# Performance work log

Measured on AMD Instinct MI355X. Metric: run time of the kernel, lower is better.

The kernel has to match this reference:

```python
import jax, jax.numpy as jnp
import numpy as np

NEG_SLOPE = 0.01  # nn.LeakyReLU default
EM_DIM = 64

def setup_inputs() -> dict:
    key = jax.random.key(0)
    k1, k2, k3, k4, k5 = jax.random.split(key, 5)
    B, N, D = 4, 512, EM_DIM
    embeddings = jax.random.normal(k1, (B, N, D), dtype=jnp.float32)
    # att_W: Linear(D, D) -> weight [D, D], bias [D]
    W_w = jax.random.normal(k2, (D, D), dtype=jnp.float32) * (1.0 / np.sqrt(D))
    W_b = jax.random.normal(k3, (D,), dtype=jnp.float32) * 0.01
    # att_a: Linear(3D, 1) -> weight [3D], bias scalar
    a_w = jax.random.normal(k4, (3 * D,), dtype=jnp.float32) * (1.0 / np.sqrt(3 * D))
    a_b = jax.random.normal(k5, (1,), dtype=jnp.float32) * 0.01
    return {"embeddings": embeddings, "W_w": W_w, "W_b": W_b, "a_w": a_w, "a_b": a_b}

def reference(embeddings, W_w, W_b, a_w, a_b):
    # embeddings: [B, N, D]
    D = embeddings.shape[-1]
    # pairwise elementwise product: value[b,i,j,d] = e[b,i,d] * e[b,j,d]
    value = embeddings[:, :, None, :] * embeddings[:, None, :, :]  # [B,N,N,D]
    # att_W applied to (broadcast) query/key is row/col-constant -> compute once per node
    w_e = jnp.einsum('bnd,ed->bne', embeddings, W_w) + W_b   # [B,N,D] (= wq rows = wk cols)
    wv = jnp.einsum('bijd,ed->bije', value, W_w) + W_b       # [B,N,N,D]
    # att_a on concat(wq, wk, wv): split the weight vector into three D-chunks
    a_q, a_k, a_v = a_w[:D], a_w[D:2*D], a_w[2*D:]
    s_q = w_e @ a_q  # [B,N]
    s_k = w_e @ a_k  # [B,N]
    s = s_q[:, :, None] + s_k[:, None, :] + jnp.einsum('bije,e->bij', wv, a_v) + a_b[0]  # [B,N,N]
    s = jnp.where(s >= 0, s, NEG_SLOPE * s)  # LeakyReLU; dropout is identity in eval
    alphas = jax.nn.softmax(s, axis=-1)[..., None]  # [B,N,N,1]
    return alphas, value
```

## Files before the change

kernel.cpp:

```cpp
#include <hip/hip_runtime.h>

#define DD 64
#define NN 512
#define BB 4
#define NEG_SLOPE 0.01f

typedef float floatx4 __attribute__((ext_vector_type(4)));

__global__ void precompute_kernel(const float* __restrict__ W_w,
                                  const float* __restrict__ W_b,
                                  const float* __restrict__ a_w,
                                  const float* __restrict__ a_b,
                                  float* __restrict__ ws) {
    int d = threadIdx.x;
    float cq = 0.f, ck = 0.f, cv = 0.f;
    for (int e = 0; e < DD; ++e) {
        float w = W_w[e * DD + d];
        cq = fmaf(a_w[e], w, cq);
        ck = fmaf(a_w[DD + e], w, ck);
        cv = fmaf(a_w[2 * DD + e], w, cv);
    }
    ws[d] = cq;
    ws[DD + d] = ck;
    ws[2 * DD + d] = cv;
    float p = W_b[d] * (a_w[d] + a_w[DD + d] + a_w[2 * DD + d]);
#pragma unroll
    for (int off = 32; off; off >>= 1) p += __shfl_down(p, off, 64);
    if (d == 0) ws[3 * DD] = p + a_b[0];
}

__global__ __launch_bounds__(256) void value_kernel(
        const float* __restrict__ emb,
        float* __restrict__ out_value) {
    const int row = blockIdx.x;
    const int b = row >> 9;
    const int t = threadIdx.x;
    const int d4 = t & 15;
    const int jl = t >> 4;

    const floatx4* emb4 = (const floatx4*)emb;
    const floatx4 ei = emb4[(size_t)row * 16 + d4];
    const floatx4* embB = emb4 + (size_t)b * NN * 16;
    floatx4* val4 = (floatx4*)out_value + (size_t)row * NN * 16;

#pragma unroll 8
    for (int it = 0; it < NN / 16; ++it) {
        const int j = it * 16 + jl;
        const floatx4 ej = embB[j * 16 + d4];
        const floatx4 p = ei * ej;
        __builtin_nontemporal_store(p, &val4[j * 16 + d4]);
    }
}

__global__ __launch_bounds__(256) void alpha_kernel(
        const float* __restrict__ emb,
        const float* __restrict__ ws,
        float* __restrict__ out_alpha) {
    const int row = blockIdx.x;
    const int b = row >> 9;
    const int t = threadIdx.x;
    const int d4 = t & 15;
    const int jl = t >> 4;

    __shared__ float s_lds[NN];
    __shared__ float red[8];

    const floatx4* emb4 = (const floatx4*)emb;
    const floatx4 ei = emb4[(size_t)row * 16 + d4];
    const floatx4 cq = ((const floatx4*)ws)[d4];
    const floatx4 ck = ((const floatx4*)(ws + DD))[d4];
    const floatx4 cv = ((const floatx4*)(ws + 2 * DD))[d4];
    const float Cc = ws[3 * DD];

    const floatx4* embB = emb4 + (size_t)b * NN * 16;

    floatx4 cvec = ei * cv + ck;
    const float pq = ei.x * cq.x + ei.y * cq.y + ei.z * cq.z + ei.w * cq.w;

#pragma unroll 4
    for (int it = 0; it < NN / 16; ++it) {
        const int j = it * 16 + jl;
        const floatx4 ej = embB[j * 16 + d4];
        float v = ej.x * cvec.x + ej.y * cvec.y + ej.z * cvec.z + ej.w * cvec.w + pq;
        v += __shfl_xor(v, 1, 64);
        v += __shfl_xor(v, 2, 64);
        v += __shfl_xor(v, 4, 64);
        v += __shfl_xor(v, 8, 64);
        if (d4 == 0) {
            float s = v + Cc;
            s_lds[j] = (s >= 0.f) ? s : NEG_SLOPE * s;
        }
    }
    __syncthreads();

    float s0 = s_lds[t], s1 = s_lds[t + 256];
    float m = fmaxf(s0, s1);
#pragma unroll
    for (int off = 32; off; off >>= 1) m = fmaxf(m, __shfl_xor(m, off, 64));
    const int wid = t >> 6, lane = t & 63;
    if (lane == 0) red[wid] = m;
    __syncthreads();
    m = fmaxf(fmaxf(red[0], red[1]), fmaxf(red[2], red[3]));

    float e0 = expf(s0 - m), e1 = expf(s1 - m);
    float ps = e0 + e1;
#pragma unroll
    for (int off = 32; off; off >>= 1) ps += __shfl_xor(ps, off, 64);
    if (lane == 0) red[4 + wid] = ps;
    __syncthreads();
    const float inv = 1.f / (red[4] + red[5] + red[6] + red[7]);

    float* arow = out_alpha + (size_t)row * NN;
    arow[t] = e0 * inv;
    arow[t + 256] = e1 * inv;
}

extern "C" void kernel_launch(void* const* d_in, const int* in_sizes, int n_in,
                              void* d_out, int out_size, void* d_ws, size_t ws_size,
                              hipStream_t stream) {
    const float* emb = (const float*)d_in[0];
    const float* W_w = (const float*)d_in[1];
    const float* W_b = (const float*)d_in[2];
    const float* a_w = (const float*)d_in[3];
    const float* a_b = (const float*)d_in[4];
    float* ws = (float*)d_ws;

    float* out = (float*)d_out;
    float* out_alpha = out;
    float* out_value = out + (size_t)BB * NN * NN;

    value_kernel<<<BB * NN, 256, 0, stream>>>(emb, out_value);
    precompute_kernel<<<1, 64, 0, stream>>>(W_w, W_b, a_w, a_b, ws);
    alpha_kernel<<<BB * NN, 256, 0, stream>>>(emb, ws, out_alpha);
}
```

Before: 302.5 us.

## Fuse value and alpha kernels into one pass with LDS partial-sum reduction

Merges the value-writing kernel and the attention-score kernel into a single kernel so each block loads the neighbor embeddings once and writes both the value tile and the scores. Per-lane partial dot products go into a padded LDS array and are summed after a barrier, instead of a shuffle reduction in the loop. This removes a launch and a second read of the embeddings. In exchange it uses about 34KB of LDS per block, which may limit occupancy, and it drops the nontemporal hint on the large value stores.

```diff
diff --git a/kernel.cpp b/kernel.cpp
--- a/kernel.cpp
+++ b/kernel.cpp
@@ -29,8 +29,10 @@
     if (d == 0) ws[3 * DD] = p + a_b[0];
 }
 
-__global__ __launch_bounds__(256) void value_kernel(
+__global__ __launch_bounds__(256) void fused_kernel(
         const float* __restrict__ emb,
+        const float* __restrict__ ws,
+        float* __restrict__ out_alpha,
         float* __restrict__ out_value) {
     const int row = blockIdx.x;
     const int b = row >> 9;
@@ -38,31 +40,7 @@
     const int d4 = t & 15;
     const int jl = t >> 4;
 
-    const floatx4* emb4 = (const floatx4*)emb;
-    const floatx4 ei = emb4[(size_t)row * 16 + d4];
-    const floatx4* embB = emb4 + (size_t)b * NN * 16;
-    floatx4* val4 = (floatx4*)out_value + (size_t)row * NN * 16;
-
-#pragma unroll 8
-    for (int it = 0; it < NN / 16; ++it) {
-        const int j = it * 16 + jl;
-        const floatx4 ej = embB[j * 16 + d4];
-        const floatx4 p = ei * ej;
-        __builtin_nontemporal_store(p, &val4[j * 16 + d4]);
-    }
-}
-
-__global__ __launch_bounds__(256) void alpha_kernel(
-        const float* __restrict__ emb,
-        const float* __restrict__ ws,
-        float* __restrict__ out_alpha) {
-    const int row = blockIdx.x;
-    const int b = row >> 9;
-    const int t = threadIdx.x;
-    const int d4 = t & 15;
-    const int jl = t >> 4;
-
-    __shared__ float s_lds[NN];
+    __shared__ float s_part[NN][17];
     __shared__ float red[8];
 
     const floatx4* emb4 = (const floatx4*)emb;
@@ -73,27 +51,32 @@
     const float Cc = ws[3 * DD];
 
     const floatx4* embB = emb4 + (size_t)b * NN * 16;
+    floatx4* val4 = (floatx4*)out_value + (size_t)row * NN * 16;
 
-    floatx4 cvec = ei * cv + ck;
+    const floatx4 cvec = ei * cv + ck;
     const float pq = ei.x * cq.x + ei.y * cq.y + ei.z * cq.z + ei.w * cq.w;
 
-#pragma unroll 4
+#pragma unroll 8
     for (int it = 0; it < NN / 16; ++it) {
         const int j = it * 16 + jl;
         const floatx4 ej = embB[j * 16 + d4];
-        float v = ej.x * cvec.x + ej.y * cvec.y + ej.z * cvec.z + ej.w * cvec.w + pq;
-        v += __shfl_xor(v, 1, 64);
-        v += __shfl_xor(v, 2, 64);
-        v += __shfl_xor(v, 4, 64);
-        v += __shfl_xor(v, 8, 64);
-        if (d4 == 0) {
-            float s = v + Cc;
-            s_lds[j] = (s >= 0.f) ? s : NEG_SLOPE * s;
-        }
+        const floatx4 p = ei * ej;
+        val4[j * 16 + d4] = p;
+        s_part[j][d4] = ej.x * cvec.x + ej.y * cvec.y
+                      + ej.z * cvec.z + ej.w * cvec.w + pq;
     }
     __syncthreads();
 
-    float s0 = s_lds[t], s1 = s_lds[t + 256];
+    float s0 = 0.f, s1 = 0.f;
+#pragma unroll
+    for (int k = 0; k < 16; ++k) {
+        s0 += s_part[t][k];
+        s1 += s_part[t + 256][k];
+    }
+    s0 += Cc; s1 += Cc;
+    s0 = (s0 >= 0.f) ? s0 : NEG_SLOPE * s0;
+    s1 = (s1 >= 0.f) ? s1 : NEG_SLOPE * s1;
+
     float m = fmaxf(s0, s1);
 #pragma unroll
     for (int off = 32; off; off >>= 1) m = fmaxf(m, __shfl_xor(m, off, 64));
@@ -129,7 +112,6 @@
     float* out_alpha = out;
     float* out_value = out + (size_t)BB * NN * NN;
 
-    value_kernel<<<BB * NN, 256, 0, stream>>>(emb, out_value);
     precompute_kernel<<<1, 64, 0, stream>>>(W_w, W_b, a_w, a_b, ws);
-    alpha_kernel<<<BB * NN, 256, 0, stream>>>(emb, ws, out_alpha);
+    fused_kernel<<<BB * NN, 256, 0, stream>>>(emb, ws, out_alpha, out_value);
 }
```

New measurement: 275.4 us. 1.1x faster.
